# Kernel optimization log

Measured on AMD Instinct MI355X. Metric: run time of the kernel, lower is better.

The kernel has to match this reference:

```python
import jax, jax.numpy as jnp
import numpy as np

N = 16384      # total nodes (8 graphs x 2048)
E = 262144     # edges (avg degree 16)
TW = 25        # time_window
H = 128        # hidden_features
POS_DIM = 2
NB = 8         # number of graphs in batch
L = 6          # hidden_layer
DT = 0.01
EPS = 1e-5
MSG_IN = 2 * H + TW + POS_DIM + 1   # 284 (actual message concat width)
UPD_IN = H + H + 1                  # 257
EMB_IN = TW + POS_DIM + 1           # 28


def _lin(key, fan_in, fan_out):
    return jax.random.normal(key, (fan_in, fan_out), jnp.float32) / np.sqrt(fan_in)


def setup_inputs() -> dict:
    key = jax.random.key(0)
    ks = jax.random.split(key, 24)
    inp = {}
    inp["u"] = jax.random.normal(ks[0], (N, TW), jnp.float32)
    inp["pos"] = jax.random.uniform(ks[1], (N, 1 + POS_DIM), jnp.float32)
    inp["edge_index"] = jax.random.randint(ks[2], (2, E), 0, N)
    inp["batch"] = jnp.sort(jax.random.randint(ks[3], (N,), 0, NB))
    # embedding MLP
    inp["emb_W1"] = _lin(ks[4], EMB_IN, H); inp["emb_b1"] = jnp.zeros((H,), jnp.float32)
    inp["emb_W2"] = _lin(ks[5], H, H);      inp["emb_b2"] = jnp.zeros((H,), jnp.float32)
    # 6 GNN layers (stacked)
    inp["msg_W1"] = jax.vmap(lambda k: _lin(k, MSG_IN, H))(jax.random.split(ks[6], L))
    inp["msg_b1"] = jnp.zeros((L, H), jnp.float32)
    inp["msg_W2"] = jax.vmap(lambda k: _lin(k, H, H))(jax.random.split(ks[7], L))
    inp["msg_b2"] = jnp.zeros((L, H), jnp.float32)
    inp["upd_W1"] = jax.vmap(lambda k: _lin(k, UPD_IN, H))(jax.random.split(ks[8], L))
    inp["upd_b1"] = jnp.zeros((L, H), jnp.float32)
    inp["upd_W2"] = jax.vmap(lambda k: _lin(k, H, H))(jax.random.split(ks[9], L))
    inp["upd_b2"] = jnp.zeros((L, H), jnp.float32)
    # output CNN: Conv1d(1,8,15,s4) -> Conv1d(8,4,10,s2) -> Conv1d(4,1,10,s1)
    inp["conv1_W"] = jax.random.normal(ks[10], (8, 1, 15), jnp.float32) / np.sqrt(15)
    inp["conv1_b"] = jnp.zeros((8,), jnp.float32)
    inp["conv2_W"] = jax.random.normal(ks[11], (4, 8, 10), jnp.float32) / np.sqrt(80)
    inp["conv2_b"] = jnp.zeros((4,), jnp.float32)
    inp["conv3_W"] = jax.random.normal(ks[12], (1, 4, 10), jnp.float32) / np.sqrt(40)
    inp["conv3_b"] = jnp.zeros((1,), jnp.float32)
    return inp


def _mlp2(x, W1, b1, W2, b2):
    return jax.nn.relu(jax.nn.relu(x @ W1 + b1) @ W2 + b2)


def _instance_norm(h, batch):
    # PyG InstanceNorm (affine=False): per-graph, per-channel normalization
    cnt = jax.ops.segment_sum(jnp.ones((h.shape[0], 1), h.dtype), batch, NB)
    cnt = jnp.maximum(cnt, 1.0)
    mean = jax.ops.segment_sum(h, batch, NB) / cnt
    meansq = jax.ops.segment_sum(h * h, batch, NB) / cnt
    var = jnp.maximum(meansq - mean * mean, 0.0)
    return (h - mean[batch]) * jax.lax.rsqrt(var[batch] + EPS)


def _gnn_layer(h, u, pos_sp, variables, src, dst, batch,
               mW1, mb1, mW2, mb2, uW1, ub1, uW2, ub2):
    # message: gather endpoints, concat, 2-layer ReLU MLP  [E, MSG_IN] -> [E, H]
    m_in = jnp.concatenate([h[dst], h[src], u[dst] - u[src],
                            pos_sp[dst] - pos_sp[src], variables[dst]], axis=-1)
    msg = _mlp2(m_in, mW1, mb1, mW2, mb2)
    # mean-scatter aggregation onto target nodes
    deg = jax.ops.segment_sum(jnp.ones((src.shape[0], 1), h.dtype), dst, N)
    agg = jax.ops.segment_sum(msg, dst, N) / jnp.maximum(deg, 1.0)
    # node update MLP + residual (in_features == out_features)
    upd = _mlp2(jnp.concatenate([h, agg, variables], axis=-1), uW1, ub1, uW2, ub2)
    return _instance_norm(h + upd, batch)


def _conv1d(x, W, b, stride):
    # x: [N, C_in, L], W: [C_out, C_in, K]
    y = jax.lax.conv_general_dilated(x, W, (stride,), 'VALID',
                                     dimension_numbers=('NCH', 'OIH', 'NCH'))
    return y + b[None, :, None]


def reference(u, pos, edge_index, batch,
              emb_W1, emb_b1, emb_W2, emb_b2,
              msg_W1, msg_b1, msg_W2, msg_b2,
              upd_W1, upd_b1, upd_W2, upd_b2,
              conv1_W, conv1_b, conv2_W, conv2_b, conv3_W, conv3_b):
    variables = pos[:, 0:1]          # time variable
    pos_sp = pos[:, 1:1 + POS_DIM]   # spatial coords
    node_input = jnp.concatenate([u, pos_sp[:, 0:1], pos_sp[:, 1:2], variables], axis=-1)
    h = _mlp2(node_input, emb_W1, emb_b1, emb_W2, emb_b2)  # [N, H]
    src, dst = edge_index[0], edge_index[1]  # PyG: row 0 = source (j), row 1 = target (i)
    for l in range(L):
        h = _gnn_layer(h, u, pos_sp, variables, src, dst, batch,
                       msg_W1[l], msg_b1[l], msg_W2[l], msg_b2[l],
                       upd_W1[l], upd_b1[l], upd_W2[l], upd_b2[l])
    # output CNN: [N,1,128] -> [N,1,1]
    y = jax.nn.relu(_conv1d(h[:, None, :], conv1_W, conv1_b, 4))
    y = jax.nn.relu(_conv1d(y, conv2_W, conv2_b, 2))
    diff = _conv1d(y, conv3_W, conv3_b, 1)[:, 0, :]        # [N, 1]
    dt = jnp.cumsum(jnp.full((1, TW), DT, jnp.float32), axis=1)
    return u[:, -1:] + dt * diff                            # [N, TW]
```

## Files before the change

### kernel.cpp

```cpp
#include <hip/hip_runtime.h>

#define NN 16384
#define NE 262144
#define TWC 25
#define HC 128
#define NBC 8
#define LC 6
#define MINC 284
#define UINC 257
#define EINC 28
#define EPSC 1e-5
#define DTC 0.01f
#define SP 65

#define FMA32F(ACCF, A0, A1, A2, A3, W0, W1_)                  \
  do {                                                         \
    float wv[8] = {W0.x, W0.y, W0.z, W0.w,                     \
                   W1_.x, W1_.y, W1_.z, W1_.w};                \
    float av[4] = {A0, A1, A2, A3};                            \
    _Pragma("unroll") for (int i_ = 0; i_ < 4; ++i_)           \
      _Pragma("unroll") for (int j_ = 0; j_ < 8; ++j_)         \
        ACCF[i_][j_] = fmaf(av[i_], wv[j_], ACCF[i_][j_]);     \
  } while (0)

#define FLUSH32(ACCD, ACCF)                                    \
  do {                                                         \
    _Pragma("unroll") for (int i_ = 0; i_ < 4; ++i_)           \
      _Pragma("unroll") for (int j_ = 0; j_ < 8; ++j_) {       \
        ACCD[i_][j_] += (double)ACCF[i_][j_];                  \
        ACCF[i_][j_] = 0.f;                                    \
      }                                                        \
  } while (0)

#define KSTEP(ACCF, WV, ROW, KW)                               \
  do {                                                         \
    float a0_ = sm[(ROW) * SP + e0 + 0];                       \
    float a1_ = sm[(ROW) * SP + e0 + 1];                       \
    float a2_ = sm[(ROW) * SP + e0 + 2];                       \
    float a3_ = sm[(ROW) * SP + e0 + 3];                       \
    float4 w0_ = WV[(KW) * 32 + jg * 2];                       \
    float4 w1_ = WV[(KW) * 32 + jg * 2 + 1];                   \
    FMA32F(ACCF, a0_, a1_, a2_, a3_, w0_, w1_);                \
  } while (0)

#define KSTEPN(ACCF, WV, ROW, KW)                              \
  do {                                                         \
    float a0_ = sm[(ROW) * SP + e0 + 0];                       \
    float a1_ = sm[(ROW) * SP + e0 + 1];                       \
    float a2_ = sm[(ROW) * SP + e0 + 2];                       \
    float a3_ = sm[(ROW) * SP + e0 + 3];                       \
    float4 w0_ = WV[(KW) * 32 + jg * 2];                       \
    float4 w1_ = WV[(KW) * 32 + jg * 2 + 1];                   \
    FMA32F(ACCF, -a0_, -a1_, -a2_, -a3_, w0_, w1_);            \
  } while (0)


__global__ __launch_bounds__(256) void k_cnt(const int* __restrict__ dst,
                                             int* __restrict__ cnt) {
  int e = blockIdx.x * 256 + threadIdx.x;
  if (e < NE) atomicAdd(&cnt[dst[e]], 1);
}

__global__ __launch_bounds__(256) void k_scan(const int* __restrict__ cnt,
                                              int* __restrict__ rowptr,
                                              int* __restrict__ fill) {
  __shared__ int part[256];
  int t = threadIdx.x;
  int s = 0;
  for (int i = 0; i < 64; ++i) s += cnt[t * 64 + i];
  part[t] = s;
  __syncthreads();
  if (t == 0) {
    int r = 0;
    for (int i = 0; i < 256; ++i) { int v = part[i]; part[i] = r; r += v; }
  }
  __syncthreads();
  int r = part[t];
  for (int i = 0; i < 64; ++i) {
    int n = t * 64 + i;
    rowptr[n] = r;
    fill[n] = r;
    r += cnt[n];
  }
  if (t == 255) rowptr[NN] = r;
}

__global__ __launch_bounds__(256) void k_scatter(const int* __restrict__ src,
                                                 const int* __restrict__ dst,
                                                 int* __restrict__ fill,
                                                 int* __restrict__ srcS,
                                                 int* __restrict__ dstS) {
  int e = blockIdx.x * 256 + threadIdx.x;
  if (e < NE) {
    int d = dst[e];
    int p = atomicAdd(&fill[d], 1);
    srcS[p] = src[e];
    dstS[p] = d;
  }
}

__global__ __launch_bounds__(256) void k_rdeg(const int* __restrict__ rowptr,
                                              float* __restrict__ rdeg) {
  int n = blockIdx.x * 256 + threadIdx.x;
  if (n < NN) {
    int c = rowptr[n + 1] - rowptr[n];
    rdeg[n] = 1.0f / (float)max(c, 1);
  }
}

__global__ __launch_bounds__(256) void k_cntb(const int* __restrict__ batch,
                                              float* __restrict__ cntb) {
  int n = blockIdx.x * 256 + threadIdx.x;
  int b = (n < NN) ? batch[n] : -1;
#pragma unroll
  for (int bb = 0; bb < NBC; ++bb) {
    unsigned long long m = __ballot(b == bb);
    if ((threadIdx.x & 63) == 0 && m != 0ULL)
      atomicAdd(&cntb[bb], (float)__popcll(m));
  }
}

__global__ __launch_bounds__(256) void k_emb(
    const float* __restrict__ u, const float* __restrict__ pos,
    const float* __restrict__ W1, const float* __restrict__ b1,
    const float* __restrict__ W2, const float* __restrict__ b2,
    float* __restrict__ h) {
  __shared__ float sin_[2][EINC];
  __shared__ float shid[2][HC];
  int n0 = blockIdx.x * 2;
  int t = threadIdx.x;
  if (t < 2 * EINC) {
    int e = t / EINC, c = t - e * EINC;
    int n = n0 + e;
    float v;
    if (c < TWC) v = u[n * TWC + c];
    else if (c == TWC) v = pos[n * 3 + 1];
    else if (c == TWC + 1) v = pos[n * 3 + 2];
    else v = pos[n * 3 + 0];
    sin_[e][c] = v;
  }
  __syncthreads();
  int e = t >> 7, j = t & 127;
  double acc = (double)b1[j];
  for (int k = 0; k < EINC; ++k)
    acc = fma((double)sin_[e][k], (double)W1[k * HC + j], acc);
  shid[e][j] = fmaxf((float)acc, 0.f);
  __syncthreads();
  double acc2 = (double)b2[j];
  for (int k = 0; k < HC; ++k)
    acc2 = fma((double)shid[e][k], (double)W2[k * HC + j], acc2);
  h[(n0 + e) * HC + j] = fmaxf((float)acc2, 0.f);
}

__global__ __launch_bounds__(256) void k_node(
    const float* __restrict__ h, const float* __restrict__ u,
    const float* __restrict__ pos, const float* __restrict__ W1,
    const float* __restrict__ b1, float* __restrict__ Dv,
    float* __restrict__ Sv) {
  __shared__ float sm[156 * SP];
  const int t = threadIdx.x;
  const int n_base = blockIdx.x * 64;
  const int isS = blockIdx.y;
  const int eg = t >> 4, jg = t & 15;
  const int e0 = eg * 4, j0 = jg * 8;
  const int half = t >> 7, col = t & 127;

  for (int it = 0; it < 32; ++it) {
    int e = 2 * it + half;
    sm[col * SP + e] = h[(n_base + e) * HC + col];
  }
  for (int idx = t; idx < 64 * 28; idx += 256) {
    int e = idx / 28, c = idx - e * 28;
    int n = n_base + e;
    float v;
    if (c < TWC) v = u[n * TWC + c];
    else if (c == TWC) v = pos[n * 3 + 1];
    else if (c == TWC + 1) v = pos[n * 3 + 2];
    else v = pos[n * 3 + 0];
    sm[(128 + c) * SP + e] = v;
  }
  __syncthreads();

  float accf[4][8];
  double accd[4][8];
#pragma unroll
  for (int jj = 0; jj < 8; ++jj) {
    double bv = isS ? 0.0 : (double)b1[j0 + jj];
#pragma unroll
    for (int i = 0; i < 4; ++i) { accd[i][jj] = bv; accf[i][jj] = 0.f; }
  }

  const float4* W1v = (const float4*)W1;
  const int wb = isS ? 128 : 0;
  for (int kc = 0; kc < 128; kc += 32) {
#pragma unroll
    for (int kk = 0; kk < 32; ++kk) KSTEP(accf, W1v, kc + kk, wb + kc + kk);
    FLUSH32(accd, accf);
  }
  if (!isS) {
#pragma unroll
    for (int kk = 0; kk < 28; ++kk) KSTEP(accf, W1v, 128 + kk, 256 + kk);
  } else {
#pragma unroll
    for (int kk = 0; kk < 27; ++kk) KSTEPN(accf, W1v, 128 + kk, 256 + kk);
  }
  FLUSH32(accd, accf);

  float* outp = isS ? Sv : Dv;
#pragma unroll
  for (int i = 0; i < 4; ++i) {
    int n = n_base + e0 + i;
#pragma unroll
    for (int jj = 0; jj < 8; ++jj)
      outp[n * HC + j0 + jj] = (float)accd[i][jj];
  }
}

__global__ __launch_bounds__(256) void k_msg(
    const float* __restrict__ Dv, const float* __restrict__ Sv,
    const int* __restrict__ srcS, const int* __restrict__ dstS,
    const float* __restrict__ W2, const float* __restrict__ b2,
    float* __restrict__ agg) {
  __shared__ float sm[128 * SP];
  const int t = threadIdx.x;
  const int e_base = blockIdx.x * 64;
  const int eg = t >> 4, jg = t & 15;
  const int e0 = eg * 4, j0 = jg * 8;
  const int half = t >> 7, col = t & 127;

  if (t < 64) {
    sm[t * SP + 64] = __int_as_float(dstS[e_base + t]);
    sm[(64 + t) * SP + 64] = __int_as_float(srcS[e_base + t]);
  }
  __syncthreads();

  for (int it = 0; it < 32; ++it) {
    int e = 2 * it + half;
    int nd = __float_as_int(sm[e * SP + 64]);
    int ns = __float_as_int(sm[(64 + e) * SP + 64]);
    sm[col * SP + e] = fmaxf(Dv[nd * HC + col] + Sv[ns * HC + col], 0.f);
  }
  __syncthreads();

  float accf[4][8];
  double accd[4][8];
#pragma unroll
  for (int jj = 0; jj < 8; ++jj) {
    double bv = (double)b2[j0 + jj];
#pragma unroll
    for (int i = 0; i < 4; ++i) { accd[i][jj] = bv; accf[i][jj] = 0.f; }
  }

  const float4* W2v = (const float4*)W2;
  for (int kc = 0; kc < 128; kc += 32) {
#pragma unroll
    for (int kk = 0; kk < 32; ++kk) KSTEP(accf, W2v, kc + kk, kc + kk);
    FLUSH32(accd, accf);
  }
  __syncthreads();

#pragma unroll
  for (int jj = 0; jj < 8; ++jj) {
#pragma unroll
    for (int i = 0; i < 4; ++i)
      sm[(j0 + jj) * SP + e0 + i] = fmaxf((float)accd[i][jj], 0.f);
  }
  __syncthreads();

  {
    int j = t & 127;
    int ebeg = (t >> 7) * 32;
    float s = 0.f;
    int cur = __float_as_int(sm[ebeg * SP + 64]);
    for (int e = ebeg; e < ebeg + 32; ++e) {
      int d = __float_as_int(sm[e * SP + 64]);
      if (d != cur) {
        atomicAdd(&agg[cur * HC + j], s);
        s = 0.f;
        cur = d;
      }
      s += sm[j * SP + e];
    }
    atomicAdd(&agg[cur * HC + j], s);
  }
}

__global__ __launch_bounds__(256) void k_upd(
    const float* __restrict__ h, const float* __restrict__ pos,
    const float* __restrict__ agg, const float* __restrict__ rdeg,
    const float* __restrict__ W1, const float* __restrict__ b1,
    const float* __restrict__ W2, const float* __restrict__ b2,
    float* __restrict__ hn) {
  __shared__ float sm[129 * SP];
  const int t = threadIdx.x;
  const int n_base = blockIdx.x * 64;
  const int eg = t >> 4, jg = t & 15;
  const int e0 = eg * 4, j0 = jg * 8;
  const int half = t >> 7, col = t & 127;

  float accf[4][8];
  double accd[4][8];
#pragma unroll
  for (int jj = 0; jj < 8; ++jj) {
    double bv = (double)b1[j0 + jj];
#pragma unroll
    for (int i = 0; i < 4; ++i) { accd[i][jj] = bv; accf[i][jj] = 0.f; }
  }

  for (int it = 0; it < 32; ++it) {
    int e = 2 * it + half;
    sm[col * SP + e] = h[(n_base + e) * HC + col];
  }
  __syncthreads();

  const float4* W1v = (const float4*)W1;
  for (int kc = 0; kc < 128; kc += 32) {
#pragma unroll
    for (int kk = 0; kk < 32; ++kk) KSTEP(accf, W1v, kc + kk, kc + kk);
    FLUSH32(accd, accf);
  }
  __syncthreads();

  for (int it = 0; it < 32; ++it) {
    int e = 2 * it + half;
    int n = n_base + e;
    sm[col * SP + e] = agg[n * HC + col] * rdeg[n];
  }
  if (t < 64) sm[128 * SP + t] = pos[(n_base + t) * 3 + 0];
  __syncthreads();

  for (int kc = 0; kc < 128; kc += 32) {
#pragma unroll
    for (int kk = 0; kk < 32; ++kk) KSTEP(accf, W1v, kc + kk, 128 + kc + kk);
    FLUSH32(accd, accf);
  }
  KSTEP(accf, W1v, 128, 256);
  FLUSH32(accd, accf);
  __syncthreads();

#pragma unroll
  for (int jj = 0; jj < 8; ++jj) {
#pragma unroll
    for (int i = 0; i < 4; ++i)
      sm[(j0 + jj) * SP + e0 + i] = fmaxf((float)accd[i][jj], 0.f);
  }
  __syncthreads();

#pragma unroll
  for (int jj = 0; jj < 8; ++jj) {
    double bv = (double)b2[j0 + jj];
#pragma unroll
    for (int i = 0; i < 4; ++i) { accd[i][jj] = bv; accf[i][jj] = 0.f; }
  }
  const float4* W2v = (const float4*)W2;
  for (int kc = 0; kc < 128; kc += 32) {
#pragma unroll
    for (int kk = 0; kk < 32; ++kk) KSTEP(accf, W2v, kc + kk, kc + kk);
    FLUSH32(accd, accf);
  }

#pragma unroll
  for (int i = 0; i < 4; ++i) {
    int n = n_base + e0 + i;
#pragma unroll
    for (int jj = 0; jj < 8; ++jj) {
      int j = j0 + jj;
      hn[n * HC + j] = h[n * HC + j] + fmaxf((float)accd[i][jj], 0.f);
    }
  }
}

__global__ __launch_bounds__(256) void k_stats(const float* __restrict__ hn,
                                               const int* __restrict__ batch,
                                               double* __restrict__ stats) {
  int n0 = blockIdx.x * 32;
  int ch = threadIdx.x & 127;
  int rh = threadIdx.x >> 7;
  double s = 0.0, ss = 0.0;
  int cur = batch[n0 + rh];
  for (int r = rh; r < 32; r += 2) {
    int n = n0 + r;
    int b = batch[n];
    double v = (double)hn[n * HC + ch];
    if (b != cur) {
      atomicAdd(&stats[cur * HC + ch], s);
      atomicAdd(&stats[NBC * HC + cur * HC + ch], ss);
      s = 0.0; ss = 0.0; cur = b;
    }
    s += v;
    ss += v * v;
  }
  atomicAdd(&stats[cur * HC + ch], s);
  atomicAdd(&stats[NBC * HC + cur * HC + ch], ss);
}

__global__ __launch_bounds__(256) void k_norm(
    const float* __restrict__ hn, const int* __restrict__ batch,
    const double* __restrict__ stats, const float* __restrict__ cntb,
    float* __restrict__ hout) {
  int idx = blockIdx.x * 256 + threadIdx.x;
  int n = idx >> 7, ch = idx & 127;
  int b = batch[n];
  double c = fmax((double)cntb[b], 1.0);
  double mean = stats[b * HC + ch] / c;
  double ms = stats[NBC * HC + b * HC + ch] / c;
  double var = fmax(ms - mean * mean, 0.0);
  hout[idx] = (float)(((double)hn[idx] - mean) / sqrt(var + EPSC));
}

__global__ __launch_bounds__(64) void k_head(
    const float* __restrict__ h, const float* __restrict__ u,
    const float* __restrict__ c1W, const float* __restrict__ c1b,
    const float* __restrict__ c2W, const float* __restrict__ c2b,
    const float* __restrict__ c3W, const float* __restrict__ c3b,
    float* __restrict__ out) {
  __shared__ float hr[128];
  __shared__ float y1[8 * 29];
  __shared__ float y2[4 * 10];
  __shared__ float dv;
  int n = blockIdx.x, t = threadIdx.x;
  hr[t] = h[n * HC + t];
  hr[t + 64] = h[n * HC + 64 + t];
  __syncthreads();
  for (int idx = t; idx < 8 * 29; idx += 64) {
    int o = idx / 29, p = idx - o * 29;
    float acc = c1b[o];
    for (int q = 0; q < 15; ++q) acc = fmaf(hr[p * 4 + q], c1W[o * 15 + q], acc);
    y1[o * 29 + p] = fmaxf(acc, 0.f);
  }
  __syncthreads();
  if (t < 40) {
    int o = t / 10, p = t - o * 10;
    float acc = c2b[o];
    for (int i = 0; i < 8; ++i)
      for (int q = 0; q < 10; ++q)
        acc = fmaf(y1[i * 29 + p * 2 + q], c2W[o * 80 + i * 10 + q], acc);
    y2[o * 10 + p] = fmaxf(acc, 0.f);
  }
  __syncthreads();
  if (t == 0) {
    float acc = c3b[0];
    for (int i = 0; i < 4; ++i)
      for (int q = 0; q < 10; ++q)
        acc = fmaf(y2[i * 10 + q], c3W[i * 10 + q], acc);
    dv = acc;
  }
  __syncthreads();
  if (t < TWC) out[n * TWC + t] = u[n * TWC + 24] + DTC * (float)(t + 1) * dv;
}

extern "C" void kernel_launch(void* const* d_in, const int* in_sizes, int n_in,
                              void* d_out, int out_size, void* d_ws,
                              size_t ws_size, hipStream_t stream) {
  const float* u = (const float*)d_in[0];
  const float* pos = (const float*)d_in[1];
  const int* ei = (const int*)d_in[2];
  const int* batch = (const int*)d_in[3];
  const float* eW1 = (const float*)d_in[4];
  const float* eb1 = (const float*)d_in[5];
  const float* eW2 = (const float*)d_in[6];
  const float* eb2 = (const float*)d_in[7];
  const float* mW1 = (const float*)d_in[8];
  const float* mb1 = (const float*)d_in[9];
  const float* mW2 = (const float*)d_in[10];
  const float* mb2 = (const float*)d_in[11];
  const float* uW1 = (const float*)d_in[12];
  const float* ub1 = (const float*)d_in[13];
  const float* uW2 = (const float*)d_in[14];
  const float* ub2 = (const float*)d_in[15];
  const float* c1W = (const float*)d_in[16];
  const float* c1b = (const float*)d_in[17];
  const float* c2W = (const float*)d_in[18];
  const float* c2b = (const float*)d_in[19];
  const float* c3W = (const float*)d_in[20];
  const float* c3b = (const float*)d_in[21];
  float* out = (float*)d_out;

  const int* srcI = ei;
  const int* dstI = ei + NE;

  double* statsd = (double*)d_ws;
  float* h = (float*)(statsd + 2 * NBC * HC);
  float* Sv = h + NN * HC;
  float* agg = Sv + NN * HC;
  float* Dhn = agg + NN * HC;
  float* rdeg = Dhn + NN * HC;
  float* cntb = rdeg + NN;
  int* cnt = (int*)(cntb + NBC);
  int* rowptr = cnt + NN;
  int* fill = rowptr + NN + 1;
  int* srcS = fill + NN;
  int* dstS = srcS + NE;

  hipMemsetAsync(cnt, 0, NN * sizeof(int), stream);
  hipMemsetAsync(cntb, 0, NBC * sizeof(float), stream);
  k_cnt<<<NE / 256, 256, 0, stream>>>(dstI, cnt);
  k_scan<<<1, 256, 0, stream>>>(cnt, rowptr, fill);
  k_scatter<<<NE / 256, 256, 0, stream>>>(srcI, dstI, fill, srcS, dstS);
  k_rdeg<<<NN / 256, 256, 0, stream>>>(rowptr, rdeg);
  k_cntb<<<NN / 256, 256, 0, stream>>>(batch, cntb);
  k_emb<<<NN / 2, 256, 0, stream>>>(u, pos, eW1, eb1, eW2, eb2, h);

  for (int l = 0; l < LC; ++l) {
    hipMemsetAsync(agg, 0, (size_t)NN * HC * sizeof(float), stream);
    hipMemsetAsync(statsd, 0, 2 * NBC * HC * sizeof(double), stream);
    k_node<<<dim3(NN / 64, 2), 256, 0, stream>>>(
        h, u, pos, mW1 + (size_t)l * MINC * HC, mb1 + l * HC, Dhn, Sv);
    k_msg<<<NE / 64, 256, 0, stream>>>(Dhn, Sv, srcS, dstS,
                                       mW2 + (size_t)l * HC * HC, mb2 + l * HC,
                                       agg);
    k_upd<<<NN / 64, 256, 0, stream>>>(h, pos, agg, rdeg,
                                       uW1 + (size_t)l * UINC * HC, ub1 + l * HC,
                                       uW2 + (size_t)l * HC * HC, ub2 + l * HC,
                                       Dhn);
    k_stats<<<NN / 32, 256, 0, stream>>>(Dhn, batch, statsd);
    k_norm<<<NN * HC / 256, 256, 0, stream>>>(Dhn, batch, statsd, cntb, h);
  }
  k_head<<<NN, 64, 0, stream>>>(h, u, c1W, c1b, c2W, c2b, c3W, c3b, out);
}
```

Baseline: 2.140 ms.

## Use packed float2 FMAs in GEMM microkernels and merge node D/S blocks

Replaces the scalar fp32 FMA inner loops with 2-wide vector FMAs that can lower to packed v_pk_fma_f32 instructions on CDNA, halving the FMA instruction count in all tiled matmuls. The node kernel now computes both the destination and source projections in one block instead of two blocks per tile, so the staged smem tile is loaded once. This also halves the grid for k_node, which reduces parallelism and adds register pressure.

```diff
diff --git a/kernel.cpp b/kernel.cpp
--- a/kernel.cpp
+++ b/kernel.cpp
@@ -13,45 +13,57 @@
 #define DTC 0.01f
 #define SP 65
 
-#define FMA32F(ACCF, A0, A1, A2, A3, W0, W1_)                  \
-  do {                                                         \
-    float wv[8] = {W0.x, W0.y, W0.z, W0.w,                     \
-                   W1_.x, W1_.y, W1_.z, W1_.w};                \
-    float av[4] = {A0, A1, A2, A3};                            \
-    _Pragma("unroll") for (int i_ = 0; i_ < 4; ++i_)           \
-      _Pragma("unroll") for (int j_ = 0; j_ < 8; ++j_)         \
-        ACCF[i_][j_] = fmaf(av[i_], wv[j_], ACCF[i_][j_]);     \
+typedef float v2f __attribute__((ext_vector_type(2)));
+
+#define KSTEPP(ACCF, WV, ROW, KW)                                        \
+  do {                                                                   \
+    v2f a01_ = {sm[(ROW) * SP + e0 + 0], sm[(ROW) * SP + e0 + 1]};       \
+    v2f a23_ = {sm[(ROW) * SP + e0 + 2], sm[(ROW) * SP + e0 + 3]};       \
+    float4 w0_ = WV[(KW) * 32 + jg * 2];                                 \
+    float4 w1_ = WV[(KW) * 32 + jg * 2 + 1];                             \
+    float wv_[8] = {w0_.x, w0_.y, w0_.z, w0_.w,                          \
+                    w1_.x, w1_.y, w1_.z, w1_.w};                         \
+    _Pragma("unroll") for (int j_ = 0; j_ < 8; ++j_) {                   \
+      v2f ws_ = {wv_[j_], wv_[j_]};                                      \
+      ACCF[0][j_] = __builtin_elementwise_fma(a01_, ws_, ACCF[0][j_]);   \
+      ACCF[1][j_] = __builtin_elementwise_fma(a23_, ws_, ACCF[1][j_]);   \
+    }                                                                    \
   } while (0)
 
-#define FLUSH32(ACCD, ACCF)                                    \
-  do {                                                         \
-    _Pragma("unroll") for (int i_ = 0; i_ < 4; ++i_)           \
-      _Pragma("unroll") for (int j_ = 0; j_ < 8; ++j_) {       \
-        ACCD[i_][j_] += (double)ACCF[i_][j_];                  \
-        ACCF[i_][j_] = 0.f;                                    \
-      }                                                        \
+#define KSTEPPN(ACCF, WV, ROW, KW)                                       \
+  do {                                                                   \
+    v2f a01_ = {sm[(ROW) * SP + e0 + 0], sm[(ROW) * SP + e0 + 1]};       \
+    v2f a23_ = {sm[(ROW) * SP + e0 + 2], sm[(ROW) * SP + e0 + 3]};       \
+    a01_ = -a01_; a23_ = -a23_;                                          \
+    float4 w0_ = WV[(KW) * 32 + jg * 2];                                 \
+    float4 w1_ = WV[(KW) * 32 + jg * 2 + 1];                             \
+    float wv_[8] = {w0_.x, w0_.y, w0_.z, w0_.w,                          \
+                    w1_.x, w1_.y, w1_.z, w1_.w};                         \
+    _Pragma("unroll") for (int j_ = 0; j_ < 8; ++j_) {                   \
+      v2f ws_ = {wv_[j_], wv_[j_]};                                      \
+      ACCF[0][j_] = __builtin_elementwise_fma(a01_, ws_, ACCF[0][j_]);   \
+      ACCF[1][j_] = __builtin_elementwise_fma(a23_, ws_, ACCF[1][j_]);   \
+    }                                                                    \
   } while (0)
 
-#define KSTEP(ACCF, WV, ROW, KW)                               \
-  do {                                                         \
-    float a0_ = sm[(ROW) * SP + e0 + 0];                       \
-    float a1_ = sm[(ROW) * SP + e0 + 1];                       \
-    float a2_ = sm[(ROW) * SP + e0 + 2];                       \
-    float a3_ = sm[(ROW) * SP + e0 + 3];                       \
-    float4 w0_ = WV[(KW) * 32 + jg * 2];                       \
-    float4 w1_ = WV[(KW) * 32 + jg * 2 + 1];                   \
-    FMA32F(ACCF, a0_, a1_, a2_, a3_, w0_, w1_);                \
+#define FLUSH32P(ACCD, ACCF)                                             \
+  do {                                                                   \
+    _Pragma("unroll") for (int i_ = 0; i_ < 4; ++i_)                     \
+      _Pragma("unroll") for (int j_ = 0; j_ < 8; ++j_)                   \
+        ACCD[i_][j_] += (double)ACCF[i_ >> 1][j_][i_ & 1];               \
+    _Pragma("unroll") for (int i_ = 0; i_ < 2; ++i_)                     \
+      _Pragma("unroll") for (int j_ = 0; j_ < 8; ++j_)                   \
+        ACCF[i_][j_] = (v2f){0.f, 0.f};                                  \
   } while (0)
 
-#define KSTEPN(ACCF, WV, ROW, KW)                              \
-  do {                                                         \
-    float a0_ = sm[(ROW) * SP + e0 + 0];                       \
-    float a1_ = sm[(ROW) * SP + e0 + 1];                       \
-    float a2_ = sm[(ROW) * SP + e0 + 2];                       \
-    float a3_ = sm[(ROW) * SP + e0 + 3];                       \
-    float4 w0_ = WV[(KW) * 32 + jg * 2];                       \
-    float4 w1_ = WV[(KW) * 32 + jg * 2 + 1];                   \
-    FMA32F(ACCF, -a0_, -a1_, -a2_, -a3_, w0_, w1_);            \
+#define ACC_INIT(ACCD, ACCF, BV)                                         \
+  do {                                                                   \
+    _Pragma("unroll") for (int j_ = 0; j_ < 8; ++j_) {                   \
+      double bv_ = (BV);                                                 \
+      _Pragma("unroll") for (int i_ = 0; i_ < 4; ++i_) ACCD[i_][j_] = bv_; \
+      ACCF[0][j_] = (v2f){0.f, 0.f};                                     \
+      ACCF[1][j_] = (v2f){0.f, 0.f};                                     \
+    }                                                                    \
   } while (0)
 
 
@@ -160,7 +172,6 @@
   __shared__ float sm[156 * SP];
   const int t = threadIdx.x;
   const int n_base = blockIdx.x * 64;
-  const int isS = blockIdx.y;
   const int eg = t >> 4, jg = t & 15;
   const int e0 = eg * 4, j0 = jg * 8;
   const int half = t >> 7, col = t & 127;
@@ -181,38 +192,42 @@
   }
   __syncthreads();
 
-  float accf[4][8];
+  const float4* W1v = (const float4*)W1;
+  v2f accf[2][8];
   double accd[4][8];
-#pragma unroll
-  for (int jj = 0; jj < 8; ++jj) {
-    double bv = isS ? 0.0 : (double)b1[j0 + jj];
-#pragma unroll
-    for (int i = 0; i < 4; ++i) { accd[i][jj] = bv; accf[i][jj] = 0.f; }
-  }
-
-  const float4* W1v = (const float4*)W1;
-  const int wb = isS ? 128 : 0;
+
+  ACC_INIT(accd, accf, (double)b1[j0 + j_]);
   for (int kc = 0; kc < 128; kc += 32) {
 #pragma unroll
-    for (int kk = 0; kk < 32; ++kk) KSTEP(accf, W1v, kc + kk, wb + kc + kk);
-    FLUSH32(accd, accf);
-  }
-  if (!isS) {
-#pragma unroll
-    for (int kk = 0; kk < 28; ++kk) KSTEP(accf, W1v, 128 + kk, 256 + kk);
-  } else {
-#pragma unroll
-    for (int kk = 0; kk < 27; ++kk) KSTEPN(accf, W1v, 128 + kk, 256 + kk);
-  }
-  FLUSH32(accd, accf);
-
-  float* outp = isS ? Sv : Dv;
+    for (int kk = 0; kk < 32; ++kk) KSTEPP(accf, W1v, kc + kk, kc + kk);
+    FLUSH32P(accd, accf);
+  }
+#pragma unroll
+  for (int kk = 0; kk < 28; ++kk) KSTEPP(accf, W1v, 128 + kk, 256 + kk);
+  FLUSH32P(accd, accf);
 #pragma unroll
   for (int i = 0; i < 4; ++i) {
     int n = n_base + e0 + i;
 #pragma unroll
     for (int jj = 0; jj < 8; ++jj)
-      outp[n * HC + j0 + jj] = (float)accd[i][jj];
+      Dv[n * HC + j0 + jj] = (float)accd[i][jj];
+  }
+
+  ACC_INIT(accd, accf, 0.0);
+  for (int kc = 0; kc < 128; kc += 32) {
+#pragma unroll
+    for (int kk = 0; kk < 32; ++kk) KSTEPP(accf, W1v, kc + kk, 128 + kc + kk);
+    FLUSH32P(accd, accf);
+  }
+#pragma unroll
+  for (int kk = 0; kk < 27; ++kk) KSTEPPN(accf, W1v, 128 + kk, 256 + kk);
+  FLUSH32P(accd, accf);
+#pragma unroll
+  for (int i = 0; i < 4; ++i) {
+    int n = n_base + e0 + i;
+#pragma unroll
+    for (int jj = 0; jj < 8; ++jj)
+      Sv[n * HC + j0 + jj] = (float)accd[i][jj];
   }
 }
 
@@ -242,20 +257,15 @@
   }
   __syncthreads();
 
-  float accf[4][8];
+  v2f accf[2][8];
   double accd[4][8];
-#pragma unroll
-  for (int jj = 0; jj < 8; ++jj) {
-    double bv = (double)b2[j0 + jj];
-#pragma unroll
-    for (int i = 0; i < 4; ++i) { accd[i][jj] = bv; accf[i][jj] = 0.f; }
-  }
+  ACC_INIT(accd, accf, (double)b2[j0 + j_]);
 
   const float4* W2v = (const float4*)W2;
   for (int kc = 0; kc < 128; kc += 32) {
 #pragma unroll
-    for (int kk = 0; kk < 32; ++kk) KSTEP(accf, W2v, kc + kk, kc + kk);
-    FLUSH32(accd, accf);
+    for (int kk = 0; kk < 32; ++kk) KSTEPP(accf, W2v, kc + kk, kc + kk);
+    FLUSH32P(accd, accf);
   }
   __syncthreads();
 
@@ -298,14 +308,9 @@
   const int e0 = eg * 4, j0 = jg * 8;
   const int half = t >> 7, col = t & 127;
 
-  float accf[4][8];
+  v2f accf[2][8];
   double accd[4][8];
-#pragma unroll
-  for (int jj = 0; jj < 8; ++jj) {
-    double bv = (double)b1[j0 + jj];
-#pragma unroll
-    for (int i = 0; i < 4; ++i) { accd[i][jj] = bv; accf[i][jj] = 0.f; }
-  }
+  ACC_INIT(accd, accf, (double)b1[j0 + j_]);
 
   for (int it = 0; it < 32; ++it) {
     int e = 2 * it + half;
@@ -316,8 +321,8 @@
   const float4* W1v = (const float4*)W1;
   for (int kc = 0; kc < 128; kc += 32) {
 #pragma unroll
-    for (int kk = 0; kk < 32; ++kk) KSTEP(accf, W1v, kc + kk, kc + kk);
-    FLUSH32(accd, accf);
+    for (int kk = 0; kk < 32; ++kk) KSTEPP(accf, W1v, kc + kk, kc + kk);
+    FLUSH32P(accd, accf);
   }
   __syncthreads();
 
@@ -331,11 +336,11 @@
 
   for (int kc = 0; kc < 128; kc += 32) {
 #pragma unroll
-    for (int kk = 0; kk < 32; ++kk) KSTEP(accf, W1v, kc + kk, 128 + kc + kk);
-    FLUSH32(accd, accf);
-  }
-  KSTEP(accf, W1v, 128, 256);
-  FLUSH32(accd, accf);
+    for (int kk = 0; kk < 32; ++kk) KSTEPP(accf, W1v, kc + kk, 128 + kc + kk);
+    FLUSH32P(accd, accf);
+  }
+  KSTEPP(accf, W1v, 128, 256);
+  FLUSH32P(accd, accf);
   __syncthreads();
 
 #pragma unroll
@@ -346,17 +351,12 @@
   }
   __syncthreads();
 
-#pragma unroll
-  for (int jj = 0; jj < 8; ++jj) {
-    double bv = (double)b2[j0 + jj];
-#pragma unroll
-    for (int i = 0; i < 4; ++i) { accd[i][jj] = bv; accf[i][jj] = 0.f; }
-  }
+  ACC_INIT(accd, accf, (double)b2[j0 + j_]);
   const float4* W2v = (const float4*)W2;
   for (int kc = 0; kc < 128; kc += 32) {
 #pragma unroll
-    for (int kk = 0; kk < 32; ++kk) KSTEP(accf, W2v, kc + kk, kc + kk);
-    FLUSH32(accd, accf);
+    for (int kk = 0; kk < 32; ++kk) KSTEPP(accf, W2v, kc + kk, kc + kk);
+    FLUSH32P(accd, accf);
   }
 
 #pragma unroll
@@ -504,7 +504,7 @@
   for (int l = 0; l < LC; ++l) {
     hipMemsetAsync(agg, 0, (size_t)NN * HC * sizeof(float), stream);
     hipMemsetAsync(statsd, 0, 2 * NBC * HC * sizeof(double), stream);
-    k_node<<<dim3(NN / 64, 2), 256, 0, stream>>>(
+    k_node<<<NN / 64, 256, 0, stream>>>(
         h, u, pos, mW1 + (size_t)l * MINC * HC, mb1 + l * HC, Dhn, Sv);
     k_msg<<<NE / 64, 256, 0, stream>>>(Dhn, Sv, srcS, dstS,
                                        mW2 + (size_t)l * HC * HC, mb2 + l * HC,
```

Measured after the change: 2.253 ms. 1.05x slower.
